# Kernel tuning notes

Hardware: AMD Instinct MI355X
Metric: run time of the kernel (lower is better)

The kernel has to match this reference:

```python
import jax, jax.numpy as jnp
import numpy as np

N, H, W = 512, 256, 256


def setup_inputs() -> dict:
    key = jax.random.key(0)
    k1, k2, k3, k4 = jax.random.split(key, 4)
    means3D = jax.random.normal(k1, (N, 3), dtype=jnp.float32) * 2.0
    A = jax.random.normal(k2, (N, 3, 3), dtype=jnp.float32) * 0.1
    covs3d = jnp.einsum('nij,nkj->nik', A, A) + 1e-4 * jnp.eye(3, dtype=jnp.float32)
    colors = jax.random.uniform(k3, (N, 3), dtype=jnp.float32)
    opacities = jax.random.uniform(k4, (N,), dtype=jnp.float32)
    fx = fy = 500.0
    K = jnp.array([[fx, 0.0, W / 2.0], [0.0, fy, H / 2.0], [0.0, 0.0, 1.0]], dtype=jnp.float32)
    R = jnp.eye(3, dtype=jnp.float32)
    t = jnp.array([0.0, 0.0, 10.0], dtype=jnp.float32)
    y, x = jnp.meshgrid(jnp.arange(H, dtype=jnp.float32), jnp.arange(W, dtype=jnp.float32), indexing='ij')
    pixels = jnp.stack([x, y], axis=-1)  # [H, W, 2]
    return dict(means3D=means3D, covs3d=covs3d, colors=colors, opacities=opacities, K=K, R=R, t=t, pixels=pixels)


def reference(means3D, covs3d, colors, opacities, K, R, t, pixels):
    # --- projection ---
    cam = means3D @ R.T + t[None, :]            # [N,3]
    depths = jnp.clip(cam[:, 2], 1.0)           # clamp(min=1.0)
    screen = cam @ K.T
    means2D = screen[:, :2] / screen[:, 2:3]    # [N,2]
    fx, fy = K[0, 0], K[1, 1]
    X, Y, Z = cam[:, 0], cam[:, 1], cam[:, 2]
    zeros = jnp.zeros_like(Z)
    # Jacobian of perspective projection, [N,2,3]
    J = jnp.stack([
        jnp.stack([fx / Z, zeros, -fx * X / (Z * Z)], axis=-1),
        jnp.stack([zeros, fy / Z, -fy * Y / (Z * Z)], axis=-1),
    ], axis=1)
    covs_cam = jnp.einsum('ij,njk,lk->nil', R, covs3d, R)     # R C R^T
    covs2D = jnp.einsum('nij,njk,nlk->nil', J, covs_cam, J)   # [N,2,2]

    # --- depth sort + validity ---
    valid = (depths > 1.0) & (depths < 50.0)
    idx = jnp.argsort(depths)
    means2D = means2D[idx]
    covs2D = covs2D[idx]
    colors_s = colors[idx]
    opac_s = opacities[idx]
    valid = valid[idx]

    # --- per-pixel gaussian values (explicit 2x2 inverse/det) ---
    covs2D = covs2D + 1e-4 * jnp.eye(2, dtype=covs2D.dtype)
    a, b = covs2D[:, 0, 0], covs2D[:, 0, 1]
    c, d = covs2D[:, 1, 0], covs2D[:, 1, 1]
    det = a * d - b * c
    ia, ib, ic, id_ = d / det, -b / det, -c / det, a / det
    dx = pixels[None, :, :, :] - means2D[:, None, None, :]    # [N,H,W,2]
    dx0, dx1 = dx[..., 0], dx[..., 1]
    expo = -0.5 * (ia[:, None, None] * dx0 * dx0
                   + (ib + ic)[:, None, None] * dx0 * dx1
                   + id_[:, None, None] * dx1 * dx1)
    norm = 1.0 / (2.0 * jnp.pi * jnp.sqrt(det))
    gauss = norm[:, None, None] * jnp.exp(expo)               # [N,H,W]
    gauss = gauss * valid[:, None, None].astype(gauss.dtype)

    # --- alpha compositing front-to-back ---
    alphas = opac_s[:, None, None] * gauss                    # [N,H,W]
    T = jnp.cumprod(1.0 - alphas, axis=0)
    T = jnp.concatenate([jnp.ones((1, H, W), dtype=alphas.dtype), T[:-1]], axis=0)
    weights = alphas * T
    rendered = jnp.einsum('nhw,nc->hwc', weights, colors_s)   # [H,W,3]
    return rendered
```

## Files before the change

### kernel.cpp

```cpp
#include <hip/hip_runtime.h>
#include <math.h>

#define N_G   512
#define W_IMG 256
#define H_IMG 256


__global__ __launch_bounds__(1024) void gs_fused(
    const float* __restrict__ means3D, const float* __restrict__ covs3d,
    const float* __restrict__ colors,  const float* __restrict__ opac,
    const float* __restrict__ Km, const float* __restrict__ Rm,
    const float* __restrict__ tv, float* __restrict__ out)
{
    __shared__ unsigned int s_key[N_G];
    __shared__ float4 s_params[N_G * 3];
    __shared__ float4 s_p[N_G * 3];
    __shared__ float4 s_part[3 * 256];
    __shared__ int    s_cnt[8];
    __shared__ int    s_off[9];

    const int tid  = threadIdx.x;
    const int wave = tid >> 6;
    const int lane = tid & 63;
    const int x0 = blockIdx.x * 16;
    const int y0 = blockIdx.y * 16;

    float mx=0.f, my=0.f, qa=0.f, qb=0.f, qd=0.f, wv=0.f, r2cut=-1.f;
    float cr=0.f, cg=0.f, cb=0.f;
    unsigned int kb = 0u;

    if (tid < N_G) {
        const int t = tid;
        const float R00=Rm[0],R01=Rm[1],R02=Rm[2],
                    R10=Rm[3],R11=Rm[4],R12=Rm[5],
                    R20=Rm[6],R21=Rm[7],R22=Rm[8];
        const float K00=Km[0],K01=Km[1],K02=Km[2],
                    K10=Km[3],K11=Km[4],K12=Km[5],
                    K20=Km[6],K21=Km[7],K22=Km[8];
        const float t0=tv[0],t1=tv[1],t2=tv[2];

        const float m0=means3D[3*t], m1=means3D[3*t+1], m2=means3D[3*t+2];
        const float cx = R00*m0 + R01*m1 + R02*m2 + t0;
        const float cy = R10*m0 + R11*m1 + R12*m2 + t1;
        const float cz = R20*m0 + R21*m1 + R22*m2 + t2;
        const float depth = fmaxf(cz, 1.0f);

        const float s0 = K00*cx + K01*cy + K02*cz;
        const float s1 = K10*cx + K11*cy + K12*cz;
        const float s2 = K20*cx + K21*cy + K22*cz;
        mx = s0 / s2;
        my = s1 / s2;

        const float C00=covs3d[9*t+0], C01=covs3d[9*t+1], C02=covs3d[9*t+2];
        const float C10=covs3d[9*t+3], C11=covs3d[9*t+4], C12=covs3d[9*t+5];
        const float C20=covs3d[9*t+6], C21=covs3d[9*t+7], C22=covs3d[9*t+8];

        const float T00 = R00*C00 + R01*C10 + R02*C20;
        const float T01 = R00*C01 + R01*C11 + R02*C21;
        const float T02 = R00*C02 + R01*C12 + R02*C22;
        const float T10 = R10*C00 + R11*C10 + R12*C20;
        const float T11 = R10*C01 + R11*C11 + R12*C21;
        const float T12 = R10*C02 + R11*C12 + R12*C22;
        const float T20 = R20*C00 + R21*C10 + R22*C20;
        const float T21 = R20*C01 + R21*C11 + R22*C21;
        const float T22 = R20*C02 + R21*C12 + R22*C22;

        const float cc00 = T00*R00 + T01*R01 + T02*R02;
        const float cc01 = T00*R10 + T01*R11 + T02*R12;
        const float cc02 = T00*R20 + T01*R21 + T02*R22;
        const float cc10 = T10*R00 + T11*R01 + T12*R02;
        const float cc11 = T10*R10 + T11*R11 + T12*R12;
        const float cc12 = T10*R20 + T11*R21 + T12*R22;
        const float cc20 = T20*R00 + T21*R01 + T22*R02;
        const float cc21 = T20*R10 + T21*R11 + T22*R12;
        const float cc22 = T20*R20 + T21*R21 + T22*R22;

        const float fx = K00, fy = K11;
        const float invz = 1.0f / cz;
        const float J00 = fx * invz;
        const float J02 = -fx * cx * invz * invz;
        const float J11 = fy * invz;
        const float J12 = -fy * cy * invz * invz;

        const float U00 = J00*cc00 + J02*cc20;
        const float U01 = J00*cc01 + J02*cc21;
        const float U02 = J00*cc02 + J02*cc22;
        const float U10 = J11*cc10 + J12*cc20;
        const float U11 = J11*cc11 + J12*cc21;
        const float U12 = J11*cc12 + J12*cc22;

        const float a = U00*J00 + U02*J02 + 1e-4f;
        const float b = U01*J11 + U02*J12;
        const float c = U10*J00 + U12*J02;
        const float d = U11*J11 + U12*J12 + 1e-4f;

        const float det = a*d - b*c;
        const float ia  = d / det;
        const float id_ = a / det;
        const float sib = (b + c) / det;

        qa = -0.5f * ia;
        qb =  0.5f * sib;
        qd = -0.5f * id_;

        const bool valid = (depth > 1.0f) && (depth < 50.0f);
        const float norm = 0.15915494309189535f * rsqrtf(det);
        wv = valid ? opac[t] * norm : 0.0f;
        if (!(wv > 0.0f)) wv = 0.0f;

        const float hm  = 0.5f * (ia + id_);
        const float dh  = 0.5f * (ia - id_);
        const float off = 0.5f * sib;
        const float lmin = hm - sqrtf(dh*dh + off*off);

        if (wv <= 1e-7f)       r2cut = -1.0f;
        else if (lmin <= 0.f)  r2cut = 1e30f;
        else                   r2cut = 2.0f * __logf(wv * 1e7f) / lmin;

        cr = colors[3*t]; cg = colors[3*t+1]; cb = colors[3*t+2];

        kb = __float_as_uint(depth);
        s_key[t] = kb;
    }
    __syncthreads();

    if (tid < N_G) {
        int rank = 0;
        const uint4* k4 = (const uint4*)s_key;
        #pragma unroll 4
        for (int j = 0; j < N_G / 4; ++j) {
            const uint4 k = k4[j];
            const int base = 4*j;
            rank += (int)(k.x < kb) + (int)((k.x == kb) && (base+0 < tid));
            rank += (int)(k.y < kb) + (int)((k.y == kb) && (base+1 < tid));
            rank += (int)(k.z < kb) + (int)((k.z == kb) && (base+2 < tid));
            rank += (int)(k.w < kb) + (int)((k.w == kb) && (base+3 < tid));
        }
        s_params[rank*3+0] = make_float4(mx, my, qa, qb);
        s_params[rank*3+1] = make_float4(qd, wv, r2cut, cr);
        s_params[rank*3+2] = make_float4(cg, cb, 0.f, 0.f);
    }
    __syncthreads();

    const float rx0 = (float)x0, ry0 = (float)y0;
    const float rx1 = rx0 + 15.f, ry1 = ry0 + 15.f;

    bool pass = false;
    unsigned long long mm = 0ull;
    float4 p0c = make_float4(0,0,0,0), p1c = make_float4(0,0,0,0);

    if (tid < N_G) {
        p0c = s_params[tid*3];
        p1c = s_params[tid*3+1];
        const float w = p1c.y, rc = p1c.z;
        const float cxp = fminf(fmaxf(p0c.x, rx0), rx1);
        const float cyp = fminf(fmaxf(p0c.y, ry0), ry1);
        const float ddx = p0c.x - cxp, ddy = p0c.y - cyp;
        const float d2 = ddx*ddx + ddy*ddy;
        pass = (w > 0.f) && (d2 <= rc);
        mm = __ballot(pass);
        if (lane == 0) s_cnt[wave] = __popcll(mm);
    }
    __syncthreads();
    if (tid == 0) {
        int acc = 0;
        #pragma unroll
        for (int g = 0; g < 8; ++g) { s_off[g] = acc; acc += s_cnt[g]; }
        s_off[8] = acc;
    }
    __syncthreads();
    if (pass) {
        const int rank = __popcll(mm & ((1ull << lane) - 1ull));
        const int dst = s_off[wave] + rank;
        s_p[dst*3+0] = p0c;
        s_p[dst*3+1] = p1c;
        s_p[dst*3+2] = s_params[tid*3+2];
    }
    __syncthreads();
    const int count = s_off[8];

    const int seg = tid >> 8;
    const int pix = tid & 255;
    const float px = (float)(x0 + (pix & 15));
    const float py = (float)(y0 + (pix >> 4));

    const int j0 = (count * seg)       >> 2;
    const int j1 = (count * (seg + 1)) >> 2;

    float T = 1.f, accr = 0.f, accg = 0.f, accb = 0.f;
    #pragma unroll 4
    for (int j = j0; j < j1; ++j) {
        const float4 p0 = s_p[j*3+0];
        const float4 p1 = s_p[j*3+1];
        const float4 p2 = s_p[j*3+2];
        const float dx = px - p0.x;
        const float dy = py - p0.y;
        const float e = (p0.z*dx + p0.w*dy)*dx + p1.x*dy*dy;
        const float alpha = p1.y * __expf(e);
        const float wt = alpha * T;
        accr = fmaf(wt, p1.w, accr);
        accg = fmaf(wt, p2.x, accg);
        accb = fmaf(wt, p2.y, accb);
        T = fmaf(-alpha, T, T);
    }

    if (seg > 0) s_part[(seg-1)*256 + pix] = make_float4(accr, accg, accb, T);
    __syncthreads();

    if (seg == 0) {
        #pragma unroll
        for (int s2 = 0; s2 < 3; ++s2) {
            const float4 q = s_part[s2*256 + pix];
            accr = fmaf(T, q.x, accr);
            accg = fmaf(T, q.y, accg);
            accb = fmaf(T, q.z, accb);
            T *= q.w;
        }
        const int o = ((y0 + (pix >> 4)) * W_IMG + (x0 + (pix & 15))) * 3;
        out[o+0] = accr;
        out[o+1] = accg;
        out[o+2] = accb;
    }
}

extern "C" void kernel_launch(void* const* d_in, const int* in_sizes, int n_in,
                              void* d_out, int out_size, void* d_ws, size_t ws_size,
                              hipStream_t stream) {
    const float* means3D = (const float*)d_in[0];
    const float* covs3d  = (const float*)d_in[1];
    const float* colors  = (const float*)d_in[2];
    const float* opac    = (const float*)d_in[3];
    const float* Km      = (const float*)d_in[4];
    const float* Rm      = (const float*)d_in[5];
    const float* tv      = (const float*)d_in[6];

    hipLaunchKernelGGL(gs_fused, dim3(W_IMG/16, H_IMG/16), dim3(1024), 0, stream,
                       means3D, covs3d, colors, opac, Km, Rm, tv, (float*)d_out);
}
```

Baseline: 86.11 us.

## Split projection and depth ranking into a separate kernel before tile rendering

Moves per-Gaussian projection and rank-based depth sort out of every tile block into a single one-block kernel that writes sorted parameters to workspace. The render kernel then culls against those global parameters with 256 threads, gathers only the surviving Gaussians into LDS, and has each thread composite one pixel sequentially instead of splitting the list four ways and merging. This removes work that all 256 blocks repeated, at the cost of an extra launch, a serial dependency on a tiny one-block kernel, and lower per-block parallelism in the compositing loop.

```diff
diff --git a/kernel.cpp b/kernel.cpp
--- a/kernel.cpp
+++ b/kernel.cpp
@@ -6,190 +6,191 @@
 #define H_IMG 256
 
 
-__global__ __launch_bounds__(1024) void gs_fused(
+__global__ __launch_bounds__(512) void gs_project_rank(
     const float* __restrict__ means3D, const float* __restrict__ covs3d,
     const float* __restrict__ colors,  const float* __restrict__ opac,
     const float* __restrict__ Km, const float* __restrict__ Rm,
-    const float* __restrict__ tv, float* __restrict__ out)
+    const float* __restrict__ tv, float4* __restrict__ params_out)
 {
     __shared__ unsigned int s_key[N_G];
-    __shared__ float4 s_params[N_G * 3];
-    __shared__ float4 s_p[N_G * 3];
-    __shared__ float4 s_part[3 * 256];
+
+    const int t = threadIdx.x;
+
+    const float R00=Rm[0],R01=Rm[1],R02=Rm[2],
+                R10=Rm[3],R11=Rm[4],R12=Rm[5],
+                R20=Rm[6],R21=Rm[7],R22=Rm[8];
+    const float K00=Km[0],K01=Km[1],K02=Km[2],
+                K10=Km[3],K11=Km[4],K12=Km[5],
+                K20=Km[6],K21=Km[7],K22=Km[8];
+    const float t0=tv[0],t1=tv[1],t2=tv[2];
+
+    const float m0=means3D[3*t], m1=means3D[3*t+1], m2=means3D[3*t+2];
+    const float cx = R00*m0 + R01*m1 + R02*m2 + t0;
+    const float cy = R10*m0 + R11*m1 + R12*m2 + t1;
+    const float cz = R20*m0 + R21*m1 + R22*m2 + t2;
+    const float depth = fmaxf(cz, 1.0f);
+
+    const float s0 = K00*cx + K01*cy + K02*cz;
+    const float s1 = K10*cx + K11*cy + K12*cz;
+    const float s2 = K20*cx + K21*cy + K22*cz;
+    const float mx = s0 / s2;
+    const float my = s1 / s2;
+
+    const float C00=covs3d[9*t+0], C01=covs3d[9*t+1], C02=covs3d[9*t+2];
+    const float C10=covs3d[9*t+3], C11=covs3d[9*t+4], C12=covs3d[9*t+5];
+    const float C20=covs3d[9*t+6], C21=covs3d[9*t+7], C22=covs3d[9*t+8];
+
+    float T00 = R00*C00 + R01*C10 + R02*C20;
+    float T01 = R00*C01 + R01*C11 + R02*C21;
+    float T02 = R00*C02 + R01*C12 + R02*C22;
+    float T10 = R10*C00 + R11*C10 + R12*C20;
+    float T11 = R10*C01 + R11*C11 + R12*C21;
+    float T12 = R10*C02 + R11*C12 + R12*C22;
+    float T20 = R20*C00 + R21*C10 + R22*C20;
+    float T21 = R20*C01 + R21*C11 + R22*C21;
+    float T22 = R20*C02 + R21*C12 + R22*C22;
+
+    const float cc00 = T00*R00 + T01*R01 + T02*R02;
+    const float cc01 = T00*R10 + T01*R11 + T02*R12;
+    const float cc02 = T00*R20 + T01*R21 + T02*R22;
+    const float cc10 = T10*R00 + T11*R01 + T12*R02;
+    const float cc11 = T10*R10 + T11*R11 + T12*R12;
+    const float cc12 = T10*R20 + T11*R21 + T12*R22;
+    const float cc20 = T20*R00 + T21*R01 + T22*R02;
+    const float cc21 = T20*R10 + T21*R11 + T22*R12;
+    const float cc22 = T20*R20 + T21*R21 + T22*R22;
+
+    const float fx = K00, fy = K11;
+    const float invz = 1.0f / cz;
+    const float J00 = fx * invz;
+    const float J02 = -fx * cx * invz * invz;
+    const float J11 = fy * invz;
+    const float J12 = -fy * cy * invz * invz;
+
+    const float U00 = J00*cc00 + J02*cc20;
+    const float U01 = J00*cc01 + J02*cc21;
+    const float U02 = J00*cc02 + J02*cc22;
+    const float U10 = J11*cc10 + J12*cc20;
+    const float U11 = J11*cc11 + J12*cc21;
+    const float U12 = J11*cc12 + J12*cc22;
+
+    const float a = U00*J00 + U02*J02 + 1e-4f;
+    const float b = U01*J11 + U02*J12;
+    const float c = U10*J00 + U12*J02;
+    const float d = U11*J11 + U12*J12 + 1e-4f;
+
+    const float det = a*d - b*c;
+    const float ia  = d / det;
+    const float id_ = a / det;
+    const float sib = (b + c) / det;
+
+    const float qa = -0.5f * ia;
+    const float qb =  0.5f * sib;
+    const float qd = -0.5f * id_;
+
+    const bool valid = (depth > 1.0f) && (depth < 50.0f);
+    const float norm = 0.15915494309189535f * rsqrtf(det);
+    float w = valid ? opac[t] * norm : 0.0f;
+    if (!(w > 0.0f)) w = 0.0f;
+
+    const float hm  = 0.5f * (ia + id_);
+    const float dh  = 0.5f * (ia - id_);
+    const float off = 0.5f * sib;
+    const float lmin = hm - sqrtf(dh*dh + off*off);
+
+    float r2cut;
+    if (w <= 1e-7f)        r2cut = -1.0f;
+    else if (lmin <= 0.f)  r2cut = 1e30f;
+    else                   r2cut = 2.0f * __logf(w * 1e7f) / lmin;
+
+    const unsigned int kb = __float_as_uint(depth);
+    s_key[t] = kb;
+    __syncthreads();
+
+    int rank = 0;
+    const uint4* k4 = (const uint4*)s_key;
+    #pragma unroll 4
+    for (int j = 0; j < N_G / 4; ++j) {
+        const uint4 k = k4[j];
+        const int base = 4*j;
+        rank += (int)(k.x < kb) + (int)((k.x == kb) && (base+0 < t));
+        rank += (int)(k.y < kb) + (int)((k.y == kb) && (base+1 < t));
+        rank += (int)(k.z < kb) + (int)((k.z == kb) && (base+2 < t));
+        rank += (int)(k.w < kb) + (int)((k.w == kb) && (base+3 < t));
+    }
+
+    params_out[rank*3+0] = make_float4(mx, my, qa, qb);
+    params_out[rank*3+1] = make_float4(qd, w, r2cut, colors[3*t]);
+    params_out[rank*3+2] = make_float4(colors[3*t+1], colors[3*t+2], 0.f, 0.f);
+}
+
+__global__ __launch_bounds__(256) void gs_render(
+    const float4* __restrict__ params, float* __restrict__ out)
+{
     __shared__ int    s_cnt[8];
     __shared__ int    s_off[9];
+    __shared__ int    s_idx[N_G];
+    __shared__ float4 s_p[N_G * 3];
 
     const int tid  = threadIdx.x;
     const int wave = tid >> 6;
     const int lane = tid & 63;
     const int x0 = blockIdx.x * 16;
     const int y0 = blockIdx.y * 16;
-
-    float mx=0.f, my=0.f, qa=0.f, qb=0.f, qd=0.f, wv=0.f, r2cut=-1.f;
-    float cr=0.f, cg=0.f, cb=0.f;
-    unsigned int kb = 0u;
-
-    if (tid < N_G) {
-        const int t = tid;
-        const float R00=Rm[0],R01=Rm[1],R02=Rm[2],
-                    R10=Rm[3],R11=Rm[4],R12=Rm[5],
-                    R20=Rm[6],R21=Rm[7],R22=Rm[8];
-        const float K00=Km[0],K01=Km[1],K02=Km[2],
-                    K10=Km[3],K11=Km[4],K12=Km[5],
-                    K20=Km[6],K21=Km[7],K22=Km[8];
-        const float t0=tv[0],t1=tv[1],t2=tv[2];
-
-        const float m0=means3D[3*t], m1=means3D[3*t+1], m2=means3D[3*t+2];
-        const float cx = R00*m0 + R01*m1 + R02*m2 + t0;
-        const float cy = R10*m0 + R11*m1 + R12*m2 + t1;
-        const float cz = R20*m0 + R21*m1 + R22*m2 + t2;
-        const float depth = fmaxf(cz, 1.0f);
-
-        const float s0 = K00*cx + K01*cy + K02*cz;
-        const float s1 = K10*cx + K11*cy + K12*cz;
-        const float s2 = K20*cx + K21*cy + K22*cz;
-        mx = s0 / s2;
-        my = s1 / s2;
-
-        const float C00=covs3d[9*t+0], C01=covs3d[9*t+1], C02=covs3d[9*t+2];
-        const float C10=covs3d[9*t+3], C11=covs3d[9*t+4], C12=covs3d[9*t+5];
-        const float C20=covs3d[9*t+6], C21=covs3d[9*t+7], C22=covs3d[9*t+8];
-
-        const float T00 = R00*C00 + R01*C10 + R02*C20;
-        const float T01 = R00*C01 + R01*C11 + R02*C21;
-        const float T02 = R00*C02 + R01*C12 + R02*C22;
-        const float T10 = R10*C00 + R11*C10 + R12*C20;
-        const float T11 = R10*C01 + R11*C11 + R12*C21;
-        const float T12 = R10*C02 + R11*C12 + R12*C22;
-        const float T20 = R20*C00 + R21*C10 + R22*C20;
-        const float T21 = R20*C01 + R21*C11 + R22*C21;
-        const float T22 = R20*C02 + R21*C12 + R22*C22;
-
-        const float cc00 = T00*R00 + T01*R01 + T02*R02;
-        const float cc01 = T00*R10 + T01*R11 + T02*R12;
-        const float cc02 = T00*R20 + T01*R21 + T02*R22;
-        const float cc10 = T10*R00 + T11*R01 + T12*R02;
-        const float cc11 = T10*R10 + T11*R11 + T12*R12;
-        const float cc12 = T10*R20 + T11*R21 + T12*R22;
-        const float cc20 = T20*R00 + T21*R01 + T22*R02;
-        const float cc21 = T20*R10 + T21*R11 + T22*R12;
-        const float cc22 = T20*R20 + T21*R21 + T22*R22;
-
-        const float fx = K00, fy = K11;
-        const float invz = 1.0f / cz;
-        const float J00 = fx * invz;
-        const float J02 = -fx * cx * invz * invz;
-        const float J11 = fy * invz;
-        const float J12 = -fy * cy * invz * invz;
-
-        const float U00 = J00*cc00 + J02*cc20;
-        const float U01 = J00*cc01 + J02*cc21;
-        const float U02 = J00*cc02 + J02*cc22;
-        const float U10 = J11*cc10 + J12*cc20;
-        const float U11 = J11*cc11 + J12*cc21;
-        const float U12 = J11*cc12 + J12*cc22;
-
-        const float a = U00*J00 + U02*J02 + 1e-4f;
-        const float b = U01*J11 + U02*J12;
-        const float c = U10*J00 + U12*J02;
-        const float d = U11*J11 + U12*J12 + 1e-4f;
-
-        const float det = a*d - b*c;
-        const float ia  = d / det;
-        const float id_ = a / det;
-        const float sib = (b + c) / det;
-
-        qa = -0.5f * ia;
-        qb =  0.5f * sib;
-        qd = -0.5f * id_;
-
-        const bool valid = (depth > 1.0f) && (depth < 50.0f);
-        const float norm = 0.15915494309189535f * rsqrtf(det);
-        wv = valid ? opac[t] * norm : 0.0f;
-        if (!(wv > 0.0f)) wv = 0.0f;
-
-        const float hm  = 0.5f * (ia + id_);
-        const float dh  = 0.5f * (ia - id_);
-        const float off = 0.5f * sib;
-        const float lmin = hm - sqrtf(dh*dh + off*off);
-
-        if (wv <= 1e-7f)       r2cut = -1.0f;
-        else if (lmin <= 0.f)  r2cut = 1e30f;
-        else                   r2cut = 2.0f * __logf(wv * 1e7f) / lmin;
-
-        cr = colors[3*t]; cg = colors[3*t+1]; cb = colors[3*t+2];
-
-        kb = __float_as_uint(depth);
-        s_key[t] = kb;
-    }
-    __syncthreads();
-
-    if (tid < N_G) {
-        int rank = 0;
-        const uint4* k4 = (const uint4*)s_key;
-        #pragma unroll 4
-        for (int j = 0; j < N_G / 4; ++j) {
-            const uint4 k = k4[j];
-            const int base = 4*j;
-            rank += (int)(k.x < kb) + (int)((k.x == kb) && (base+0 < tid));
-            rank += (int)(k.y < kb) + (int)((k.y == kb) && (base+1 < tid));
-            rank += (int)(k.z < kb) + (int)((k.z == kb) && (base+2 < tid));
-            rank += (int)(k.w < kb) + (int)((k.w == kb) && (base+3 < tid));
-        }
-        s_params[rank*3+0] = make_float4(mx, my, qa, qb);
-        s_params[rank*3+1] = make_float4(qd, wv, r2cut, cr);
-        s_params[rank*3+2] = make_float4(cg, cb, 0.f, 0.f);
-    }
-    __syncthreads();
-
     const float rx0 = (float)x0, ry0 = (float)y0;
     const float rx1 = rx0 + 15.f, ry1 = ry0 + 15.f;
 
-    bool pass = false;
-    unsigned long long mm = 0ull;
-    float4 p0c = make_float4(0,0,0,0), p1c = make_float4(0,0,0,0);
-
-    if (tid < N_G) {
-        p0c = s_params[tid*3];
-        p1c = s_params[tid*3+1];
-        const float w = p1c.y, rc = p1c.z;
-        const float cxp = fminf(fmaxf(p0c.x, rx0), rx1);
-        const float cyp = fminf(fmaxf(p0c.y, ry0), ry1);
-        const float ddx = p0c.x - cxp, ddy = p0c.y - cyp;
+    bool pass[2];
+    unsigned long long mm[2];
+    int gix[2];
+    #pragma unroll
+    for (int cgrp = 0; cgrp < 2; ++cgrp) {
+        const int g = wave + 4 * cgrp;
+        const int i = g * 64 + lane;
+        gix[cgrp] = i;
+        const float4 p0 = params[i*3];
+        const float4 p1 = params[i*3+1];
+        const float w = p1.y, r2cut = p1.z;
+        const float cxp = fminf(fmaxf(p0.x, rx0), rx1);
+        const float cyp = fminf(fmaxf(p0.y, ry0), ry1);
+        const float ddx = p0.x - cxp, ddy = p0.y - cyp;
         const float d2 = ddx*ddx + ddy*ddy;
-        pass = (w > 0.f) && (d2 <= rc);
-        mm = __ballot(pass);
-        if (lane == 0) s_cnt[wave] = __popcll(mm);
+        pass[cgrp] = (w > 0.f) && (d2 <= r2cut);
+        mm[cgrp] = __ballot(pass[cgrp]);
+        if (lane == 0) s_cnt[g] = __popcll(mm[cgrp]);
     }
     __syncthreads();
     if (tid == 0) {
         int acc = 0;
-        #pragma unroll
         for (int g = 0; g < 8; ++g) { s_off[g] = acc; acc += s_cnt[g]; }
         s_off[8] = acc;
     }
     __syncthreads();
-    if (pass) {
-        const int rank = __popcll(mm & ((1ull << lane) - 1ull));
-        const int dst = s_off[wave] + rank;
-        s_p[dst*3+0] = p0c;
-        s_p[dst*3+1] = p1c;
-        s_p[dst*3+2] = s_params[tid*3+2];
+    #pragma unroll
+    for (int cgrp = 0; cgrp < 2; ++cgrp) {
+        const int g = wave + 4 * cgrp;
+        if (pass[cgrp]) {
+            const int rank = __popcll(mm[cgrp] & ((1ull << lane) - 1ull));
+            s_idx[s_off[g] + rank] = gix[cgrp];
+        }
     }
     __syncthreads();
     const int count = s_off[8];
 
-    const int seg = tid >> 8;
-    const int pix = tid & 255;
-    const float px = (float)(x0 + (pix & 15));
-    const float py = (float)(y0 + (pix >> 4));
-
-    const int j0 = (count * seg)       >> 2;
-    const int j1 = (count * (seg + 1)) >> 2;
-
+    for (int j = tid; j < count; j += 256) {
+        const int gi = s_idx[j];
+        s_p[j*3+0] = params[gi*3+0];
+        s_p[j*3+1] = params[gi*3+1];
+        s_p[j*3+2] = params[gi*3+2];
+    }
+    __syncthreads();
+
+    const float px = (float)(x0 + (tid & 15));
+    const float py = (float)(y0 + (tid >> 4));
     float T = 1.f, accr = 0.f, accg = 0.f, accb = 0.f;
+
     #pragma unroll 4
-    for (int j = j0; j < j1; ++j) {
+    for (int j = 0; j < count; ++j) {
         const float4 p0 = s_p[j*3+0];
         const float4 p1 = s_p[j*3+1];
         const float4 p2 = s_p[j*3+2];
@@ -204,23 +205,10 @@
         T = fmaf(-alpha, T, T);
     }
 
-    if (seg > 0) s_part[(seg-1)*256 + pix] = make_float4(accr, accg, accb, T);
-    __syncthreads();
-
-    if (seg == 0) {
-        #pragma unroll
-        for (int s2 = 0; s2 < 3; ++s2) {
-            const float4 q = s_part[s2*256 + pix];
-            accr = fmaf(T, q.x, accr);
-            accg = fmaf(T, q.y, accg);
-            accb = fmaf(T, q.z, accb);
-            T *= q.w;
-        }
-        const int o = ((y0 + (pix >> 4)) * W_IMG + (x0 + (pix & 15))) * 3;
-        out[o+0] = accr;
-        out[o+1] = accg;
-        out[o+2] = accb;
-    }
+    const int o = ((y0 + (tid >> 4)) * W_IMG + (x0 + (tid & 15))) * 3;
+    out[o+0] = accr;
+    out[o+1] = accg;
+    out[o+2] = accb;
 }
 
 extern "C" void kernel_launch(void* const* d_in, const int* in_sizes, int n_in,
@@ -234,6 +222,11 @@
     const float* Rm      = (const float*)d_in[5];
     const float* tv      = (const float*)d_in[6];
 
-    hipLaunchKernelGGL(gs_fused, dim3(W_IMG/16, H_IMG/16), dim3(1024), 0, stream,
-                       means3D, covs3d, colors, opac, Km, Rm, tv, (float*)d_out);
+    float4* params = (float4*)d_ws;
+    float*  out    = (float*)d_out;
+
+    hipLaunchKernelGGL(gs_project_rank, dim3(1), dim3(512), 0, stream,
+                       means3D, covs3d, colors, opac, Km, Rm, tv, params);
+    hipLaunchKernelGGL(gs_render, dim3(16, 16), dim3(256), 0, stream,
+                       params, out);
 }
```

Measured after the change: 89.47 us. 3.9% more time.
